# Kernel optimization log

Hardware: AMD Instinct MI355X
Metric: run time of the kernel (lower is better)

## Reference

```python
import jax, jax.numpy as jnp
import numpy as np

B = 65536       # batch
F_SUB = 128     # sub-6GHz features
F_MM = 128      # mmWave features (pairs of real/imag)
H = 512         # hidden size (all three MLPs)
C = 64          # class_num (beams)
WB_SEL = 8      # number of selected wideband beams


def _mlp(x, w1, b1, w2, b2, wd, bd):
    # MLP with do_bn=False, dropout=0: Linear->ReLU->Linear->ReLU->Linear
    h = jax.nn.relu(x @ w1 + b1)
    h = jax.nn.relu(h @ w2 + b2)
    return h @ wd + bd


def setup_inputs() -> dict:
    key = jax.random.key(0)
    ks = jax.random.split(key, 16)
    w = lambda k, shape: (jax.random.normal(k, shape, jnp.float32) * 0.02)
    z = lambda n: jnp.zeros((n,), jnp.float32)
    return {
        "x": jax.random.normal(ks[0], (B, F_SUB), jnp.float32),
        "y": jax.random.normal(ks[1], (B, F_MM), jnp.float32),
        "sub_w1": w(ks[2], (F_SUB, H)), "sub_b1": z(H),
        "sub_w2": w(ks[3], (H, H)),     "sub_b2": z(H),
        "sub_wd": w(ks[4], (H, C)),     "sub_bd": z(C),
        "mm_w1": w(ks[5], (F_MM, H)),   "mm_b1": z(H),
        "mm_w2": w(ks[6], (H, H)),      "mm_b2": z(H),
        "mm_wd": w(ks[7], (H, C)),      "mm_bd": z(C),
        "att_w": w(ks[8], (2 * C, 2 * C)), "att_b": z(2 * C),
        "fus_w1": w(ks[9], (2 * C, H)), "fus_b1": z(H),
        "fus_w2": w(ks[10], (H, H)),    "fus_b2": z(H),
        "fus_wd": w(ks[11], (H, C)),    "fus_bd": z(C),
        "wb_sel": WB_SEL,
    }


def reference(x, y, sub_w1, sub_b1, sub_w2, sub_b2, sub_wd, sub_bd,
              mm_w1, mm_b1, mm_w2, mm_b2, mm_wd, mm_bd,
              att_w, att_b, fus_w1, fus_b1, fus_w2, fus_b2, fus_wd, fus_bd,
              wb_sel):
    b, f_mm = y.shape
    out_sub = _mlp(x, sub_w1, sub_b1, sub_w2, sub_b2, sub_wd, sub_bd)  # [B, C]
    class_num = out_sub.shape[1]
    wb_num = (class_num * 2) // f_mm  # int(class_num / features_mm * 2)
    # beam-group scores: sum consecutive groups of wb_num logits -> [B, f_mm/2]
    p_mm = out_sub.reshape(b, class_num // wb_num, wb_num).sum(axis=2)
    # top-k selected wideband beams (indices detached in original)
    _, idx = jax.lax.top_k(p_mm, wb_sel)               # [B, wb_sel]
    # scatter-build masked mmWave input: keep (idx*2, idx*2+1) pairs, zero rest
    rows = jnp.arange(b)[:, None]                       # [B, 1]
    mask = jnp.zeros_like(y)
    mask = mask.at[rows, idx * 2].set(1.0)
    mask = mask.at[rows, idx * 2 + 1].set(1.0)
    input_mm = y * mask
    out_mm = _mlp(input_mm, mm_w1, mm_b1, mm_w2, mm_b2, mm_wd, mm_bd)  # [B, C]
    cat = jnp.concatenate([out_sub, out_mm], axis=1)    # [B, 2C]
    out_att = jax.nn.sigmoid(cat @ att_w + att_b)       # [B, 2C]
    fused = _mlp(cat * out_att, fus_w1, fus_b1, fus_w2, fus_b2, fus_wd, fus_bd)
    return (out_sub, out_mm, fused)
```

## Files before the change

kernel.cpp:

```cpp
#include <hip/hip_runtime.h>
#include <math.h>


typedef _Float16 halfx8 __attribute__((ext_vector_type(8)));
typedef float    floatx4 __attribute__((ext_vector_type(4)));
#define MFMA16(a,b,c) __builtin_amdgcn_mfma_f32_16x16x32_f16((a),(b),(c),0,0,0)

#define BN 65536
#define MROWS 32
#define MARGIN 2e-4f

#define SM_IX0 0
#define SM_IX1 8192
#define SM_H0  16384
#define SM_H1  49152
#define SM_BYTES 81920
#define OBST 66

#define SZ_W1 65536
#define SZ_W2 262144
#define SZ_WD 32768
#define SZ_ATT 16384
#define OFF_SW1 0
#define OFF_SW2 (OFF_SW1 + SZ_W1)
#define OFF_SWD (OFF_SW2 + SZ_W2)
#define OFF_MW1 (OFF_SWD + SZ_WD)
#define OFF_MW2 (OFF_MW1 + SZ_W1)
#define OFF_MWD (OFF_MW2 + SZ_W2)
#define OFF_FW1 (OFF_MWD + SZ_WD)
#define OFF_FW2 (OFF_FW1 + SZ_W1)
#define OFF_FWD (OFF_FW2 + SZ_W2)
#define OFF_ATT (OFF_FWD + SZ_WD)

#define WS_MASKS (5u << 20)
#define WS_RROWS (6u << 20)
#define WS_RCNT  (7u << 20)
#define WS_FLAGS ((7u << 20) + 256)

enum { R_X = 0, R_Y, R_SW1, R_SB1, R_SW2, R_SB2, R_SWD, R_SBD,
       R_MW1, R_MB1, R_MW2, R_MB2, R_MWD, R_MBD, R_ATTW, R_ATTB,
       R_FW1, R_FB1, R_FW2, R_FB2, R_FWD, R_FBD, N_ROLES };

__device__ __forceinline__ float bf2f(unsigned short u) {
    return __uint_as_float((unsigned)u << 16);
}
__device__ __forceinline__ float loadf(const void* p, size_t i, int fl) {
    return fl == 1 ? bf2f(((const unsigned short*)p)[i])
         : fl == 0 ? ((const float*)p)[i] : 0.f;
}
__device__ __forceinline__ double loadd(const void* p, size_t i, int fl) {
    return fl == 1 ? (double)bf2f(((const unsigned short*)p)[i])
         : fl == 0 ? (double)((const float*)p)[i] : 0.0;
}
template<int FL>
__device__ __forceinline__ double ldw(const void* p, size_t i) {
    return FL == 1 ? (double)bf2f(((const unsigned short*)p)[i])
         : FL == 0 ? (double)((const float*)p)[i] : 0.0;
}
struct hf2 { _Float16 hi, lo; };
__device__ __forceinline__ hf2 split2h(float v) {
    hf2 r;
    r.hi = (_Float16)v;
    r.lo = (_Float16)(v - (float)r.hi);
    return r;
}
__device__ __forceinline__ int swz(int row, int colB, int rsB) {
    return (row * rsB + colB) ^ ((row & 15) << 4);
}

__device__ __forceinline__ void ld_b4(const _Float16* __restrict__ p,
                                      int base, int ktn, int kt, int l,
                                      halfx8 (&b)[4])
{
#pragma unroll
    for (int nt = 0; nt < 4; ++nt) {
        const size_t fi = ((((size_t)(base + nt)) * ktn + kt) * 64 + l) * 8;
        b[nt] = *(const halfx8*)(p + fi);
    }
}

__device__ __forceinline__ void kt_mfma(const char* __restrict__ sm,
                                        int smA0, int smA1, int rsB,
                                        int kt, int l15, int q,
                                        const halfx8 (&b)[4],
                                        floatx4 (&acc)[2][4])
{
    const int cB = kt * 64 + q * 16;
    halfx8 ahi[2], alo[2];
#pragma unroll
    for (int rt = 0; rt < 2; ++rt) {
        const int off = swz(rt * 16 + l15, cB, rsB);
        ahi[rt] = *(const halfx8*)(sm + smA0 + off);
        alo[rt] = *(const halfx8*)(sm + smA1 + off);
    }
#pragma unroll
    for (int nt = 0; nt < 4; ++nt)
#pragma unroll
        for (int rt = 0; rt < 2; ++rt) {
            acc[rt][nt] = MFMA16(alo[rt], b[nt], acc[rt][nt]);
            acc[rt][nt] = MFMA16(ahi[rt], b[nt], acc[rt][nt]);
        }
}

struct DetArgs { const void* p[N_ROLES]; int n[N_ROLES]; };

__global__ __launch_bounds__(256) void detect_kernel(DetArgs da, int* flags, int* rcnt) {
    const int role = blockIdx.x;
    if (role == 0 && threadIdx.x == 0) *rcnt = 0;
    const unsigned short* u = (const unsigned short*)da.p[role];
    int nsamp = da.n[role] / 2;
    if (nsamp > 4096) nsamp = 4096;
    __shared__ int band, nz;
    if (threadIdx.x == 0) { band = 0; nz = 0; }
    __syncthreads();
    int lb = 0, lnz = 0;
    for (int i = threadIdx.x; i < nsamp; i += 256) {
        const unsigned short v = u[2 * i];
        if (v) {
            ++lnz;
            const int e = (v >> 7) & 0xFF;
            if (e >= 100 && e <= 126) ++lb;
        }
    }
    atomicAdd(&band, lb);
    atomicAdd(&nz, lnz);
    __syncthreads();
    if (threadIdx.x == 0)
        flags[role] = (nz == 0) ? 2 : ((band * 2 > nz) ? 1 : 0);
}

struct PackArgs { const void* src[10]; int K[10], N[10], off[10], role[10]; };

__global__ __launch_bounds__(256) void pack_weights(PackArgs pa, _Float16* dst,
                                                    const int* __restrict__ flags) {
    const int m = blockIdx.y;
    const int fl = flags[pa.role[m]];
    const int K = pa.K[m], N = pa.N[m];
    const int KT = K >> 5, NT = N >> 4;
    const int total = KT * NT * 64;
    const int t = blockIdx.x * 256 + threadIdx.x;
    if (t >= total) return;
    const int l = t & 63;
    const int idx = t >> 6;
    const int kt = idx % KT;
    const int nt = idx / KT;
    const int k0 = kt * 32 + ((l >> 4) << 3);
    const int n  = nt * 16 + (l & 15);
    _Float16* dh = dst + pa.off[m] + (size_t)t * 8;
#pragma unroll
    for (int j = 0; j < 8; ++j)
        dh[j] = (_Float16)loadf(pa.src[m], (size_t)(k0 + j) * N + n, fl);
}

template <bool SUB>
__device__ __forceinline__ void mlp_core(
    char* __restrict__ sm,
    const _Float16* __restrict__ p1,
    const _Float16* __restrict__ p2,
    const _Float16* __restrict__ pd,
    const void* __restrict__ b1, int fb1,
    const void* __restrict__ b2, int fb2,
    const void* __restrict__ bd, int fbd,
    int r0, float* __restrict__ out)
{
    const int tid = threadIdx.x;
    const int l = tid & 63, w = tid >> 6, l15 = l & 15, q = l >> 4;

    floatx4 acc[2][4];
#pragma unroll
    for (int rt = 0; rt < 2; ++rt)
#pragma unroll
        for (int nt = 0; nt < 4; ++nt) acc[rt][nt] = (floatx4)0.0f;
#pragma unroll
    for (int kt = 0; kt < 4; ++kt) {
        halfx8 B[4];
        ld_b4(p1, w * 4, 4, kt, l, B);
        kt_mfma(sm, SM_IX0, SM_IX1, 256, kt, l15, q, B, acc);
    }
#pragma unroll
    for (int nt = 0; nt < 4; ++nt) {
        const int col = w * 64 + nt * 16 + l15;
        const float bias = loadf(b1, col, fb1);
#pragma unroll
        for (int rt = 0; rt < 2; ++rt)
#pragma unroll
            for (int r = 0; r < 4; ++r) {
                const int row = rt * 16 + q * 4 + r;
                float v = acc[rt][nt][r] + bias;
                v = v > 0.f ? v : 0.f;
                const hf2 s = split2h(v);
                const int o = swz(row, col * 2, 1024);
                *(_Float16*)(sm + SM_H0 + o) = s.hi;
                *(_Float16*)(sm + SM_H1 + o) = s.lo;
            }
    }
    __syncthreads();

    floatx4 acc2[2][4];
#pragma unroll
    for (int rt = 0; rt < 2; ++rt)
#pragma unroll
        for (int nt = 0; nt < 4; ++nt) acc2[rt][nt] = (floatx4)0.0f;
    for (int kt = 0; kt < 16; ++kt) {
        halfx8 B[4];
        ld_b4(p2, w * 4, 16, kt, l, B);
        kt_mfma(sm, SM_H0, SM_H1, 1024, kt, l15, q, B, acc2);
    }
    __syncthreads();
#pragma unroll
    for (int nt = 0; nt < 4; ++nt) {
        const int col = w * 64 + nt * 16 + l15;
        const float bias = loadf(b2, col, fb2);
#pragma unroll
        for (int rt = 0; rt < 2; ++rt)
#pragma unroll
            for (int r = 0; r < 4; ++r) {
                const int row = rt * 16 + q * 4 + r;
                float v = acc2[rt][nt][r] + bias;
                v = v > 0.f ? v : 0.f;
                const hf2 s = split2h(v);
                const int o = swz(row, col * 2, 1024);
                *(_Float16*)(sm + SM_H0 + o) = s.hi;
                *(_Float16*)(sm + SM_H1 + o) = s.lo;
            }
    }
    __syncthreads();

    {
        const int nt3 = w & 3, rt3 = w >> 2;
        floatx4 a3 = (floatx4)0.0f;
        for (int kt = 0; kt < 16; ++kt) {
            const size_t fi = (((size_t)(nt3 * 16 + kt)) * 64 + l) * 8;
            const halfx8 b = *(const halfx8*)(pd + fi);
            const int off = swz(rt3 * 16 + l15, kt * 64 + q * 16, 1024);
            const halfx8 ahi = *(const halfx8*)(sm + SM_H0 + off);
            const halfx8 alo = *(const halfx8*)(sm + SM_H1 + off);
            a3 = MFMA16(alo, b, a3);
            a3 = MFMA16(ahi, b, a3);
        }
        const int col = nt3 * 16 + l15;
        const float bias = loadf(bd, col, fbd);
        float* outb = (float*)sm;
#pragma unroll
        for (int r = 0; r < 4; ++r) {
            const int row = rt3 * 16 + q * 4 + r;
            const float v = a3[r] + bias;
            out[(size_t)(r0 + row) * 64 + col] = v;
            if (SUB) outb[row * OBST + col] = v;
        }
    }
    if (SUB) __syncthreads();
}

__global__ __launch_bounds__(512, 4)
void sub_mfma(const void* __restrict__ x, const _Float16* __restrict__ wpack,
              const void* __restrict__ b1, const void* __restrict__ b2,
              const void* __restrict__ bd, const int* __restrict__ flags,
              float* __restrict__ out, unsigned long long* __restrict__ masks,
              int* __restrict__ rrows, int* __restrict__ rcnt)
{
    __shared__ __align__(16) char sm[SM_BYTES];
    const int fx = flags[R_X];
    const int r0 = blockIdx.x * MROWS;

    for (int i = threadIdx.x; i < MROWS * 128; i += 512) {
        const int r = i >> 7, c = i & 127;
        const hf2 s = split2h(loadf(x, (size_t)(r0 + r) * 128 + c, fx));
        const int off = swz(r, c * 2, 256);
        *(_Float16*)(sm + SM_IX0 + off) = s.hi;
        *(_Float16*)(sm + SM_IX1 + off) = s.lo;
    }
    __syncthreads();

    mlp_core<true>(sm, wpack + OFF_SW1, wpack + OFF_SW2, wpack + OFF_SWD,
                   b1, flags[R_SB1], b2, flags[R_SB2], bd, flags[R_SBD],
                   r0, out);

    if (threadIdx.x < MROWS) {
        const float* rowp = (const float*)sm + threadIdx.x * OBST;
        float vals[9];
        int idxs[9];
#pragma unroll
        for (int j = 0; j < 9; ++j) { vals[j] = -__builtin_inff(); idxs[j] = 0; }
        for (int i = 0; i < 64; ++i) {
            const float v = rowp[i];
            if (v > vals[8]) {
                int p = 8;
                while (p > 0 && v > vals[p - 1]) {
                    vals[p] = vals[p - 1];
                    idxs[p] = idxs[p - 1];
                    --p;
                }
                vals[p] = v;
                idxs[p] = i;
            }
        }
        unsigned long long m = 0ull;
#pragma unroll
        for (int j = 0; j < 8; ++j) m |= (1ull << idxs[j]);
        masks[r0 + threadIdx.x] = m;
        if (vals[7] - vals[8] < MARGIN) {
            const int slot = atomicAdd(rcnt, 1);
            rrows[slot] = r0 + threadIdx.x;
        }
    }
}

#define RPB 16
#define OBST2 66

template<int FL>
__device__ __forceinline__ void r1_layer(const void* __restrict__ W,
                                         const float* __restrict__ xs,
                                         double* __restrict__ a, int t)
{
#pragma unroll 4
    for (int k = 0; k < 128; ++k) {
        const double w = ldw<FL>(W, (size_t)k * 512 + t);
#pragma unroll
        for (int r = 0; r < RPB; ++r)
            a[r] = fma((double)xs[r * 128 + k], w, a[r]);
    }
}

template<int FL>
__device__ __forceinline__ void r2_layer(const void* __restrict__ W,
                                         const double* __restrict__ hsm,
                                         double* __restrict__ a, int t)
{
#pragma unroll 4
    for (int k = 0; k < 512; ++k) {
        const double w = ldw<FL>(W, (size_t)k * 512 + t);
        const double2* hp = (const double2*)(hsm + k * 16);
#pragma unroll
        for (int j = 0; j < 8; ++j) {
            const double2 hv = hp[j];
            a[2 * j]     = fma(hv.x, w, a[2 * j]);
            a[2 * j + 1] = fma(hv.y, w, a[2 * j + 1]);
        }
    }
}

template<int FL>
__device__ __forceinline__ void r3_layer(const void* __restrict__ W,
                                         const double* __restrict__ hsm,
                                         int c, int rg, double* __restrict__ a)
{
#pragma unroll 4
    for (int k = 0; k < 512; ++k) {
        const double w = ldw<FL>(W, (size_t)k * 64 + c);
        a[0] = fma(hsm[k * 16 + rg * 2],     w, a[0]);
        a[1] = fma(hsm[k * 16 + rg * 2 + 1], w, a[1]);
    }
}

#define R_DISPATCH(fl, CALL)                                   \
    do {                                                       \
        if ((fl) == 1)      { CALL(1); }                       \
        else if ((fl) == 0) { CALL(0); }                       \
        else                { CALL(2); }                       \
    } while (0)

__global__ __launch_bounds__(512, 4)
void rescue_kernel(const void* __restrict__ x,
                   const void* __restrict__ W1, const void* __restrict__ b1,
                   const void* __restrict__ W2, const void* __restrict__ b2,
                   const void* __restrict__ Wd, const void* __restrict__ bd,
                   const int* __restrict__ flags,
                   const int* __restrict__ rrows, const int* __restrict__ rcnt,
                   float* __restrict__ out, unsigned long long* __restrict__ masks)
{
    __shared__ int rowids[RPB];
    __shared__ __align__(16) char xob[RPB * OBST2 * 8];
    __shared__ __align__(16) double hsm[512 * RPB];
    float* xs = (float*)xob;
    double* ob = (double*)xob;
    const int fx = flags[R_X], f1 = flags[R_SW1], fb1 = flags[R_SB1],
              f2 = flags[R_SW2], fb2 = flags[R_SB2],
              f3 = flags[R_SWD], fb3 = flags[R_SBD];
    const int t = threadIdx.x;
    const int n = *rcnt;

    for (int g = blockIdx.x; g * RPB < n; g += gridDim.x) {
        const int base = g * RPB;
        int cnt = n - base;
        if (cnt > RPB) cnt = RPB;
        if (t < RPB) rowids[t] = rrows[base + (t < cnt ? t : cnt - 1)];
        __syncthreads();

        for (int i = t; i < RPB * 128; i += 512) {
            const int r = i >> 7, c = i & 127;
            xs[r * 128 + c] = loadf(x, (size_t)rowids[r] * 128 + c, fx);
        }
        __syncthreads();

        {
            double a[RPB];
#pragma unroll
            for (int r = 0; r < RPB; ++r) a[r] = 0.0;
#define L1_CALL(FL) r1_layer<FL>(W1, xs, a, t)
            R_DISPATCH(f1, L1_CALL);
#undef L1_CALL
            const double bb = loadd(b1, t, fb1);
#pragma unroll
            for (int r = 0; r < RPB; ++r) {
                const double v = a[r] + bb;
                hsm[t * 16 + r] = v > 0.0 ? v : 0.0;
            }
        }
        __syncthreads();

        {
            double a[RPB];
#pragma unroll
            for (int r = 0; r < RPB; ++r) a[r] = 0.0;
#define L2_CALL(FL) r2_layer<FL>(W2, hsm, a, t)
            R_DISPATCH(f2, L2_CALL);
#undef L2_CALL
            __syncthreads();
            const double bb = loadd(b2, t, fb2);
#pragma unroll
            for (int r = 0; r < RPB; ++r) {
                const double v = a[r] + bb;
                hsm[t * 16 + r] = v > 0.0 ? v : 0.0;
            }
        }
        __syncthreads();

        {
            const int c = t & 63, rg = t >> 6;
            double a[2];
            a[0] = 0.0;
            a[1] = 0.0;
#define L3_CALL(FL) r3_layer<FL>(Wd, hsm, c, rg, a)
            R_DISPATCH(f3, L3_CALL);
#undef L3_CALL
            const double bb = loadd(bd, c, fb3);
#pragma unroll
            for (int j = 0; j < 2; ++j) {
                const int r = rg * 2 + j;
                const double v = a[j] + bb;
                ob[r * OBST2 + c] = v;
                if (r < cnt) out[(size_t)rowids[r] * 64 + c] = (float)v;
            }
        }
        __syncthreads();

        if (t < cnt) {
            double vals[8];
            int idxs[8];
#pragma unroll
            for (int j = 0; j < 8; ++j) { vals[j] = -1.0e300; idxs[j] = 0; }
            for (int i = 0; i < 64; ++i) {
                const double v = ob[t * OBST2 + i];
                if (v > vals[7]) {
                    int p = 7;
                    while (p > 0 && v > vals[p - 1]) {
                        vals[p] = vals[p - 1];
                        idxs[p] = idxs[p - 1];
                        --p;
                    }
                    vals[p] = v;
                    idxs[p] = i;
                }
            }
            unsigned long long m = 0ull;
#pragma unroll
            for (int j = 0; j < 8; ++j) m |= (1ull << idxs[j]);
            masks[rowids[t]] = m;
        }
        __syncthreads();
    }
}

__global__ __launch_bounds__(512, 4)
void mm_mfma(const unsigned long long* __restrict__ masks,
             const void* __restrict__ y, const _Float16* __restrict__ wpack,
             const void* __restrict__ b1, const void* __restrict__ b2,
             const void* __restrict__ bd, const int* __restrict__ flags,
             float* __restrict__ out)
{
    __shared__ __align__(16) char sm[SM_BYTES];
    const int fy = flags[R_Y];
    const int r0 = blockIdx.x * MROWS;

    for (int i = threadIdx.x; i < MROWS * 128; i += 512) {
        const int r = i >> 7, c = i & 127;
        const bool keep = (masks[r0 + r] >> (c >> 1)) & 1ull;
        const float v = keep ? loadf(y, (size_t)(r0 + r) * 128 + c, fy) : 0.f;
        const hf2 s = split2h(v);
        const int off = swz(r, c * 2, 256);
        *(_Float16*)(sm + SM_IX0 + off) = s.hi;
        *(_Float16*)(sm + SM_IX1 + off) = s.lo;
    }
    __syncthreads();

    mlp_core<false>(sm, wpack + OFF_MW1, wpack + OFF_MW2, wpack + OFF_MWD,
                    b1, flags[R_MB1], b2, flags[R_MB2], bd, flags[R_MBD],
                    r0, out);
}

__global__ __launch_bounds__(512, 4)
void fusion_mfma(const float* __restrict__ subf, const float* __restrict__ mmf,
                 const _Float16* __restrict__ wpack,
                 const void* __restrict__ attb,
                 const void* __restrict__ b1, const void* __restrict__ b2,
                 const void* __restrict__ bd, const int* __restrict__ flags,
                 float* __restrict__ out)
{
    __shared__ __align__(16) char sm[SM_BYTES];
    const int tid = threadIdx.x;
    const int l = tid & 63, w = tid >> 6, l15 = l & 15, q = l >> 4;
    const int r0 = blockIdx.x * MROWS;

    for (int i = tid; i < MROWS * 128; i += 512) {
        const int r = i >> 7, c = i & 127;
        const size_t row = (size_t)(r0 + r);
        const float v = (c < 64) ? subf[row * 64 + c] : mmf[row * 64 + (c - 64)];
        const hf2 s = split2h(v);
        const int off = swz(r, c * 2, 256);
        *(_Float16*)(sm + SM_IX0 + off) = s.hi;
        *(_Float16*)(sm + SM_IX1 + off) = s.lo;
    }
    __syncthreads();

    floatx4 aacc[2];
    aacc[0] = (floatx4)0.0f;
    aacc[1] = (floatx4)0.0f;
    const _Float16* patt = wpack + OFF_ATT;
#pragma unroll
    for (int kt = 0; kt < 4; ++kt) {
        const size_t fi = (((size_t)(w * 4 + kt)) * 64 + l) * 8;
        const halfx8 b = *(const halfx8*)(patt + fi);
        const int cB = kt * 64 + q * 16;
#pragma unroll
        for (int rt = 0; rt < 2; ++rt) {
            const int off = swz(rt * 16 + l15, cB, 256);
            const halfx8 ahi = *(const halfx8*)(sm + SM_IX0 + off);
            const halfx8 alo = *(const halfx8*)(sm + SM_IX1 + off);
            aacc[rt] = MFMA16(alo, b, aacc[rt]);
            aacc[rt] = MFMA16(ahi, b, aacc[rt]);
        }
    }
    const int col = w * 16 + l15;
    const float ab = loadf(attb, col, flags[R_ATTB]);
    float gated[2][4];
#pragma unroll
    for (int rt = 0; rt < 2; ++rt)
#pragma unroll
        for (int r = 0; r < 4; ++r) {
            const int rowl = rt * 16 + q * 4 + r;
            const float pre = aacc[rt][r] + ab;
            const float s = 1.f / (1.f + expf(-pre));
            const int off = swz(rowl, col * 2, 256);
            const float catv = (float)*(const _Float16*)(sm + SM_IX0 + off)
                             + (float)*(const _Float16*)(sm + SM_IX1 + off);
            gated[rt][r] = catv * s;
        }
    __syncthreads();
#pragma unroll
    for (int rt = 0; rt < 2; ++rt)
#pragma unroll
        for (int r = 0; r < 4; ++r) {
            const int rowl = rt * 16 + q * 4 + r;
            const hf2 s = split2h(gated[rt][r]);
            const int off = swz(rowl, col * 2, 256);
            *(_Float16*)(sm + SM_IX0 + off) = s.hi;
            *(_Float16*)(sm + SM_IX1 + off) = s.lo;
        }
    __syncthreads();

    mlp_core<false>(sm, wpack + OFF_FW1, wpack + OFF_FW2, wpack + OFF_FWD,
                    b1, flags[R_FB1], b2, flags[R_FB2], bd, flags[R_FBD],
                    r0, out);
}

extern "C" void kernel_launch(void* const* d_in, const int* in_sizes, int n_in,
                              void* d_out, int out_size, void* d_ws, size_t ws_size,
                              hipStream_t stream)
{
    static const int dictSizes[23] = {8388608, 8388608, 65536, 512, 262144, 512,
                                      32768, 64, 65536, 512, 262144, 512, 32768, 64,
                                      16384, 128, 65536, 512, 262144, 512, 32768, 64, 1};
    static const int dictRole[23]  = {R_X, R_Y, R_SW1, R_SB1, R_SW2, R_SB2, R_SWD, R_SBD,
                                      R_MW1, R_MB1, R_MW2, R_MB2, R_MWD, R_MBD,
                                      R_ATTW, R_ATTB, R_FW1, R_FB1, R_FW2, R_FB2,
                                      R_FWD, R_FBD, -1};
    static const int sortSizes[23] = {128, 16384, 512, 512, 64, 65536, 262144, 32768,
                                      512, 512, 64, 65536, 262144, 32768,
                                      512, 512, 64, 65536, 262144, 32768, 1,
                                      8388608, 8388608};
    static const int sortRole[23]  = {R_ATTB, R_ATTW, R_FB1, R_FB2, R_FBD, R_FW1,
                                      R_FW2, R_FWD, R_MB1, R_MB2, R_MBD, R_MW1,
                                      R_MW2, R_MWD, R_SB1, R_SB2, R_SBD, R_SW1,
                                      R_SW2, R_SWD, -1, R_X, R_Y};
    const void* rp[N_ROLES];
    int rs[N_ROLES];
    for (int i = 0; i < 23 && i < n_in; ++i)
        if (dictRole[i] >= 0) { rp[dictRole[i]] = d_in[i]; rs[dictRole[i]] = in_sizes[i]; }
    {
        bool dictOk = (n_in >= 22);
        for (int i = 0; i < 22 && dictOk; ++i)
            if (in_sizes[i] != dictSizes[i]) dictOk = false;
        if (!dictOk) {
            bool sortOk = (n_in >= 23);
            for (int i = 0; i < 23 && sortOk; ++i)
                if (in_sizes[i] != sortSizes[i]) sortOk = false;
            if (sortOk)
                for (int i = 0; i < 23; ++i)
                    if (sortRole[i] >= 0) { rp[sortRole[i]] = d_in[i]; rs[sortRole[i]] = in_sizes[i]; }
        }
    }

    _Float16* wpack = (_Float16*)d_ws;
    unsigned long long* masks = (unsigned long long*)((char*)d_ws + WS_MASKS);
    int* rrows = (int*)((char*)d_ws + WS_RROWS);
    int* rcnt  = (int*)((char*)d_ws + WS_RCNT);
    int* flags = (int*)((char*)d_ws + WS_FLAGS);

    float* out_f = (float*)d_out;
    float* sub_o = out_f;
    float* mm_o  = out_f + (size_t)BN * 64;
    float* fus_o = out_f + (size_t)2 * BN * 64;

    DetArgs da;
    for (int r = 0; r < N_ROLES; ++r) { da.p[r] = rp[r]; da.n[r] = rs[r]; }
    detect_kernel<<<N_ROLES, 256, 0, stream>>>(da, flags, rcnt);

    PackArgs pa;
    const int prole[10] = {R_SW1, R_SW2, R_SWD, R_MW1, R_MW2, R_MWD,
                           R_FW1, R_FW2, R_FWD, R_ATTW};
    const int Ks[10]   = {128, 512, 512, 128, 512, 512, 128, 512, 512, 128};
    const int Ns[10]   = {512, 512, 64, 512, 512, 64, 512, 512, 64, 128};
    const int offs[10] = {OFF_SW1, OFF_SW2, OFF_SWD, OFF_MW1, OFF_MW2,
                          OFF_MWD, OFF_FW1, OFF_FW2, OFF_FWD, OFF_ATT};
    for (int i = 0; i < 10; ++i) {
        pa.src[i] = rp[prole[i]];
        pa.K[i] = Ks[i];
        pa.N[i] = Ns[i];
        pa.off[i] = offs[i];
        pa.role[i] = prole[i];
    }
    pack_weights<<<dim3(128, 10), 256, 0, stream>>>(pa, wpack, flags);

    sub_mfma<<<BN / MROWS, 512, 0, stream>>>(
        rp[R_X], wpack, rp[R_SB1], rp[R_SB2], rp[R_SBD], flags,
        sub_o, masks, rrows, rcnt);

    rescue_kernel<<<512, 512, 0, stream>>>(
        rp[R_X], rp[R_SW1], rp[R_SB1], rp[R_SW2], rp[R_SB2], rp[R_SWD], rp[R_SBD],
        flags, rrows, rcnt, sub_o, masks);

    mm_mfma<<<BN / MROWS, 512, 0, stream>>>(
        masks, rp[R_Y], wpack, rp[R_MB1], rp[R_MB2], rp[R_MBD], flags, mm_o);

    fusion_mfma<<<BN / MROWS, 512, 0, stream>>>(
        sub_o, mm_o, wpack, rp[R_ATTB], rp[R_FB1], rp[R_FB2], rp[R_FBD],
        flags, fus_o);
}
```

Before: 956.1 us.

## Retile rescue kernel fp64 MLP to 2 rows x 8 cols per thread with swizzled LDS

The fp64 rescue kernel that recomputes near-tie top-k rows now gives each thread 2 rows by 8 consecutive output columns instead of 16 rows by 1 column. The hidden activations in shared memory use an XOR-swizzled layout, and the input tile gets a padded stride. Together these are meant to cut LDS bank conflicts and make each wavefront read a single broadcast double2 from LDS. In exchange each thread issues 8 weight loads per k, making global weight reads less coalesced per lane. The rescue path only handles a small set of rows, so its share of total kernel time is probably minor.

```diff
diff --git a/kernel.cpp b/kernel.cpp
--- a/kernel.cpp
+++ b/kernel.cpp
@@ -307,36 +307,44 @@
 }
 
 #define RPB 16
+#define XST3 130
 #define OBST2 66
+
+__device__ __forceinline__ int hswz(int k, int r) {
+    return k * 16 + (r ^ (((k >> 3) & 7) << 1));
+}
 
 template<int FL>
 __device__ __forceinline__ void r1_layer(const void* __restrict__ W,
                                          const float* __restrict__ xs,
-                                         double* __restrict__ a, int t)
+                                         double (&a)[2][8], int w, int c0)
 {
 #pragma unroll 4
     for (int k = 0; k < 128; ++k) {
-        const double w = ldw<FL>(W, (size_t)k * 512 + t);
-#pragma unroll
-        for (int r = 0; r < RPB; ++r)
-            a[r] = fma((double)xs[r * 128 + k], w, a[r]);
+        const double x0 = (double)xs[(2 * w) * XST3 + k];
+        const double x1 = (double)xs[(2 * w + 1) * XST3 + k];
+#pragma unroll
+        for (int j = 0; j < 8; ++j) {
+            const double wv = ldw<FL>(W, (size_t)k * 512 + c0 + j);
+            a[0][j] = fma(x0, wv, a[0][j]);
+            a[1][j] = fma(x1, wv, a[1][j]);
+        }
     }
 }
 
 template<int FL>
 __device__ __forceinline__ void r2_layer(const void* __restrict__ W,
                                          const double* __restrict__ hsm,
-                                         double* __restrict__ a, int t)
-{
-#pragma unroll 4
+                                         double (&a)[2][8], int w, int c0)
+{
+#pragma unroll 2
     for (int k = 0; k < 512; ++k) {
-        const double w = ldw<FL>(W, (size_t)k * 512 + t);
-        const double2* hp = (const double2*)(hsm + k * 16);
+        const double2 hv = *(const double2*)(hsm + hswz(k, 2 * w));
 #pragma unroll
         for (int j = 0; j < 8; ++j) {
-            const double2 hv = hp[j];
-            a[2 * j]     = fma(hv.x, w, a[2 * j]);
-            a[2 * j + 1] = fma(hv.y, w, a[2 * j + 1]);
+            const double wv = ldw<FL>(W, (size_t)k * 512 + c0 + j);
+            a[0][j] = fma(hv.x, wv, a[0][j]);
+            a[1][j] = fma(hv.y, wv, a[1][j]);
         }
     }
 }
@@ -344,13 +352,14 @@
 template<int FL>
 __device__ __forceinline__ void r3_layer(const void* __restrict__ W,
                                          const double* __restrict__ hsm,
-                                         int c, int rg, double* __restrict__ a)
+                                         int c, int rg, double (&a)[2])
 {
 #pragma unroll 4
     for (int k = 0; k < 512; ++k) {
-        const double w = ldw<FL>(W, (size_t)k * 64 + c);
-        a[0] = fma(hsm[k * 16 + rg * 2],     w, a[0]);
-        a[1] = fma(hsm[k * 16 + rg * 2 + 1], w, a[1]);
+        const double2 hv = *(const double2*)(hsm + hswz(k, 2 * rg));
+        const double wv = ldw<FL>(W, (size_t)k * 64 + c);
+        a[0] = fma(hv.x, wv, a[0]);
+        a[1] = fma(hv.y, wv, a[1]);
     }
 }
 
@@ -379,6 +388,8 @@
               f2 = flags[R_SW2], fb2 = flags[R_SB2],
               f3 = flags[R_SWD], fb3 = flags[R_SBD];
     const int t = threadIdx.x;
+    const int l = t & 63, w = t >> 6;
+    const int c0 = l * 8;
     const int n = *rcnt;
 
     for (int g = blockIdx.x; g * RPB < n; g += gridDim.x) {
@@ -389,40 +400,50 @@
         __syncthreads();
 
         for (int i = t; i < RPB * 128; i += 512) {
-            const int r = i >> 7, c = i & 127;
-            xs[r * 128 + c] = loadf(x, (size_t)rowids[r] * 128 + c, fx);
+            const int r = i >> 7, k = i & 127;
+            xs[r * XST3 + k] = loadf(x, (size_t)rowids[r] * 128 + k, fx);
         }
         __syncthreads();
 
         {
-            double a[RPB];
-#pragma unroll
-            for (int r = 0; r < RPB; ++r) a[r] = 0.0;
-#define L1_CALL(FL) r1_layer<FL>(W1, xs, a, t)
+            double a[2][8];
+#pragma unroll
+            for (int rr = 0; rr < 2; ++rr)
+#pragma unroll
+                for (int j = 0; j < 8; ++j) a[rr][j] = 0.0;
+#define L1_CALL(FL) r1_layer<FL>(W1, xs, a, w, c0)
             R_DISPATCH(f1, L1_CALL);
 #undef L1_CALL
-            const double bb = loadd(b1, t, fb1);
-#pragma unroll
-            for (int r = 0; r < RPB; ++r) {
-                const double v = a[r] + bb;
-                hsm[t * 16 + r] = v > 0.0 ? v : 0.0;
+#pragma unroll
+            for (int j = 0; j < 8; ++j) {
+                const double bb = loadd(b1, c0 + j, fb1);
+#pragma unroll
+                for (int rr = 0; rr < 2; ++rr) {
+                    const double v = a[rr][j] + bb;
+                    hsm[hswz(c0 + j, 2 * w + rr)] = v > 0.0 ? v : 0.0;
+                }
             }
         }
         __syncthreads();
 
         {
-            double a[RPB];
-#pragma unroll
-            for (int r = 0; r < RPB; ++r) a[r] = 0.0;
-#define L2_CALL(FL) r2_layer<FL>(W2, hsm, a, t)
+            double a[2][8];
+#pragma unroll
+            for (int rr = 0; rr < 2; ++rr)
+#pragma unroll
+                for (int j = 0; j < 8; ++j) a[rr][j] = 0.0;
+#define L2_CALL(FL) r2_layer<FL>(W2, hsm, a, w, c0)
             R_DISPATCH(f2, L2_CALL);
 #undef L2_CALL
             __syncthreads();
-            const double bb = loadd(b2, t, fb2);
-#pragma unroll
-            for (int r = 0; r < RPB; ++r) {
-                const double v = a[r] + bb;
-                hsm[t * 16 + r] = v > 0.0 ? v : 0.0;
+#pragma unroll
+            for (int j = 0; j < 8; ++j) {
+                const double bb = loadd(b2, c0 + j, fb2);
+#pragma unroll
+                for (int rr = 0; rr < 2; ++rr) {
+                    const double v = a[rr][j] + bb;
+                    hsm[hswz(c0 + j, 2 * w + rr)] = v > 0.0 ? v : 0.0;
+                }
             }
         }
         __syncthreads();
```

Result: faster. 848.3 us (-11.3%).
